# Kernel optimization log

Measured on AMD Instinct MI355X. Metric: run time of the kernel, lower is better.

The kernel has to match this reference:

```python
import jax, jax.numpy as jnp
import numpy as np

B, T = 256, 2048
U = Y = 32
H = 128
Z = 64
L = 2  # GRU layers


def _mlp2(x, w1, b1, w2, b2):
    # Linear -> ReLU -> Linear (PyTorch Linear: y = x @ W.T + b)
    return jax.nn.relu(x @ w1.T + b1) @ w2.T + b2


def _gru_cell(x, h, wih, whh):
    # PyTorch GRUCell (bias=False), gate order [r, z, n]
    gi = x @ wih.T  # [B, 3H]
    gh = h @ whh.T
    i_r, i_z, i_n = jnp.split(gi, 3, axis=-1)
    h_r, h_z, h_n = jnp.split(gh, 3, axis=-1)
    r = jax.nn.sigmoid(i_r + h_r)
    z = jax.nn.sigmoid(i_z + h_z)
    n = jnp.tanh(i_n + r * h_n)
    return (1.0 - z) * n + z * h


def setup_inputs() -> dict:
    key = jax.random.key(0)
    ks = jax.random.split(key, 32)
    f32 = jnp.float32
    w = lambda k, shape: jax.random.normal(k, shape, f32) * 0.05
    inp = {
        'u': jax.random.normal(ks[0], (B, U, T), f32),
        'y': jax.random.normal(ks[1], (B, Y, T), f32),
        'h0': jax.random.uniform(ks[2], (L, B, H), f32),
        # phi_u: Linear(U,H) ReLU Linear(H,H)
        'pu_w1': w(ks[3], (H, U)), 'pu_b1': w(ks[4], (H,)),
        'pu_w2': w(ks[5], (H, H)), 'pu_b2': w(ks[6], (H,)),
        # dynn: Linear(2H,H) ReLU Linear(H,H)
        'dy_w1': w(ks[7], (H, 2 * H)), 'dy_b1': w(ks[8], (H,)),
        'dy_w2': w(ks[9], (H, H)), 'dy_b2': w(ks[10], (H,)),
        # x_mean / x_logvar heads: Linear(H,Z)
        'xm_w': w(ks[11], (Z, H)), 'xm_b': w(ks[12], (Z,)),
        'xlv_w': w(ks[13], (Z, H)), 'xlv_b': w(ks[14], (Z,)),
        # phi_x: Linear(2Z,H) ReLU Linear(H,H)
        'px_w1': w(ks[15], (H, 2 * Z)), 'px_b1': w(ks[16], (H,)),
        'px_w2': w(ks[17], (H, H)), 'px_b2': w(ks[18], (H,)),
        # menn: Linear(H,H) ReLU Linear(H,Y)
        'me_w1': w(ks[19], (H, H)), 'me_b1': w(ks[20], (H,)),
        'me_w2': w(ks[21], (Y, H)), 'me_b2': w(ks[22], (Y,)),
        # GRU (bias=False), stacked per layer: [L, 3H, H]
        'gru_wih': w(ks[23], (L, 3 * H, H)),
        'gru_whh': w(ks[24], (L, 3 * H, H)),
    }
    return inp


def reference(u, y, h0, pu_w1, pu_b1, pu_w2, pu_b2, dy_w1, dy_b1, dy_w2, dy_b2,
              xm_w, xm_b, xlv_w, xlv_b, px_w1, px_b1, px_w2, px_b2,
              me_w1, me_b1, me_w2, me_b2, gru_wih, gru_whh):
    u_seq = jnp.moveaxis(u, 2, 0)  # [T, B, U]
    y_seq = jnp.moveaxis(y, 2, 0)  # [T, B, Y]

    def step(carry, ty):
        h, loss = carry  # h: [L, B, H]
        ut, yt = ty
        phi_u = _mlp2(ut, pu_w1, pu_b1, pu_w2, pu_b2)                     # [B, H]
        dphi = _mlp2(jnp.concatenate([phi_u, h[-1]], axis=1),
                     dy_w1, dy_b1, dy_w2, dy_b2)                          # [B, H]
        x_mean = dphi @ xm_w.T + xm_b                                     # [B, Z]
        x_logvar = dphi @ xlv_w.T + xlv_b                                 # [B, Z]
        # GRU step (uses pre-update h; dynn already consumed old h[-1])
        inp = phi_u
        new_h = []
        for l in range(L):
            hl = _gru_cell(inp, h[l], gru_wih[l], gru_whh[l])
            new_h.append(hl)
            inp = hl
        h = jnp.stack(new_h)
        # mpnt_wt <= 0 branch: pure NN measurement
        phi_x = _mlp2(jnp.concatenate([x_mean, x_logvar], axis=1),
                      px_w1, px_b1, px_w2, px_b2)                         # [B, H]
        y_hat = _mlp2(phi_x, me_w1, me_b1, me_w2, me_b2)                  # [B, Y]
        loss = loss + jnp.sum((y_hat - yt) ** 2)
        return (h, loss), None

    (h, loss), _ = jax.lax.scan(step, (h0, jnp.float32(0.0)), (u_seq, y_seq))
    return loss
```

## Files before the change

kernel.cpp:

```cpp
#include <hip/hip_runtime.h>

#define DI __device__ __forceinline__

typedef unsigned short u16;
typedef unsigned int u32;
typedef unsigned long long u64;
typedef __bf16 bf16v __attribute__((ext_vector_type(8)));
typedef float f32x4 __attribute__((ext_vector_type(4)));

constexpr int B_ = 256, T_ = 2048, H_ = 128;
constexpr int BU = B_ * 32;

constexpr size_t O_PU_W1 = 0;
constexpr size_t O_PU_W2 = 4096;
constexpr size_t O_DY_W1 = 20480;
constexpr size_t O_DY_W2 = 53248;
constexpr size_t O_XM_W  = 69632;
constexpr size_t O_XLV_W = 77824;
constexpr size_t O_PX_W1 = 86016;
constexpr size_t O_PX_W2 = 102400;
constexpr size_t O_ME_W1 = 118784;
constexpr size_t O_ME_W2 = 135168;
constexpr size_t O_WIH   = 139264;
constexpr size_t O_WHH   = 237568;

constexpr size_t WS_WB   = 0;
constexpr size_t WS_HST  = 0x100000;
constexpr size_t WS_PART = 0x140000;
constexpr size_t WS_DATA = 0x180000;

DI u16 f2b(float x) {
  union { float f; unsigned u; } v; v.f = x;
  unsigned r = v.u + 0x7fffu + ((v.u >> 16) & 1u);
  return (u16)(r >> 16);
}
DI float b2f(u16 h) { union { unsigned u; float f; } v; v.u = ((unsigned)h) << 16; return v.f; }
DI float asf(u32 u) { union { unsigned u; float f; } v; v.u = u; return v.f; }
DI float sigm(float x) {
  return __builtin_amdgcn_rcpf(1.f + __builtin_amdgcn_exp2f(-1.44269504f * x));
}
DI float tanhg(float x) {
  return fmaf(2.f, __builtin_amdgcn_rcpf(1.f + __builtin_amdgcn_exp2f(-2.88539008f * x)), -1.f);
}
DI f32x4 MFMA(bf16v a, bf16v b, f32x4 c) {
  return __builtin_amdgcn_mfma_f32_16x16x32_bf16(a, b, c, 0, 0, 0);
}
DI void MFA(f32x4& c, const bf16v& a_agpr, const bf16v& b) {
  asm("v_mfma_f32_16x16x32_bf16 %0, %1, %2, %0"
      : "+v"(c) : "a"(a_agpr), "v"(b));
}
DI bf16v ldb(const u16* p) { return *reinterpret_cast<const bf16v*>(p); }
DI u32 cvtpk(float a, float b) {
  u32 d;
  asm("v_cvt_pk_bf16_f32 %0, %1, %2" : "=v"(d) : "v"(a), "v"(b));
  return d;
}
DI u64 pk4(float a, float b, float c, float d) {
  return (u64)cvtpk(a, b) | ((u64)cvtpk(c, d) << 32);
}
DI void bar_lds() {
  asm volatile("s_waitcnt lgkmcnt(0)\n\ts_barrier" ::: "memory");
}

__global__ void k_convert_weights(
    const float* pu_w1, const float* pu_w2, const float* dy_w1, const float* dy_w2,
    const float* xm_w, const float* xlv_w, const float* px_w1, const float* px_w2,
    const float* me_w1, const float* me_w2, const float* gih, const float* ghh,
    const float* h0, u16* wb, float* hst) {
  int i0 = blockIdx.x * blockDim.x + threadIdx.x;
  int st = gridDim.x * blockDim.x;
#define CVT(src, off, n) for (int i = i0; i < (n); i += st) wb[(off) + i] = f2b(src[i]);
  CVT(pu_w1, O_PU_W1, 4096)  CVT(pu_w2, O_PU_W2, 16384)
  CVT(dy_w1, O_DY_W1, 32768) CVT(dy_w2, O_DY_W2, 16384)
  CVT(xm_w,  O_XM_W,  8192)  CVT(xlv_w, O_XLV_W, 8192)
  CVT(px_w1, O_PX_W1, 16384) CVT(px_w2, O_PX_W2, 16384)
  CVT(me_w1, O_ME_W1, 16384) CVT(me_w2, O_ME_W2, 4096)
  CVT(gih,   O_WIH,   98304) CVT(ghh,   O_WHH,   98304)
#undef CVT
  for (int i = i0; i < 2 * B_ * H_; i += st) hst[i] = h0[i];
}

__global__ void k_transpose(const float* __restrict__ u, const float* __restrict__ y,
                            u16* __restrict__ uT, u16* __restrict__ yT, int t0) {
  const float* src = blockIdx.z ? y : u;
  u16* dst = blockIdx.z ? yT : uT;
  __shared__ float tile[32][33];
  const int tx = threadIdx.x, ty = threadIdx.y;
  const int c0 = blockIdx.x * 32;
  const int r0 = blockIdx.y * 32;
#pragma unroll
  for (int i = 0; i < 4; ++i)
    tile[ty + i * 8][tx] = src[(size_t)(r0 + ty + i * 8) * T_ + t0 + c0 + tx];
  __syncthreads();
#pragma unroll
  for (int i = 0; i < 4; ++i)
    dst[(size_t)(c0 + ty + i * 8) * BU + r0 + tx] = f2b(tile[tx][ty + i * 8]);
}

DI void role_gru(u16* smem, const u16* __restrict__ gi0, const u16* __restrict__ wb,
                 float* __restrict__ hst, u16* __restrict__ h1old, int TCr, int blk) {
  u16* SH0 = smem;
  u16* SH1 = smem + 4352;
  const int lane = threadIdx.x & 63, w = threadIdx.x >> 6;
  const int ln = lane & 15, lq = lane >> 4;
  const int f0 = w * 16;
  const int fme = f0 + lq * 4;
  const int b0 = blk * 16;
  const u16* wh0 = wb + O_WHH;
  const u16* wi1 = wb + O_WIH + 49152;
  const u16* wh1 = wb + O_WHH + 49152;

  bf16v wH0[3][4], wI1[3][4], wH1[3][4];
#pragma unroll
  for (int g = 0; g < 3; ++g)
#pragma unroll
    for (int kt = 0; kt < 4; ++kt) {
      size_t row = (size_t)(g * 128 + f0 + ln);
      size_t col = (size_t)kt * 32 + lq * 8;
      wH0[g][kt] = ldb(wh0 + row * H_ + col);
      wI1[g][kt] = ldb(wi1 + row * H_ + col);
      wH1[g][kt] = ldb(wh1 + row * H_ + col);
    }
#pragma unroll
  for (int g = 0; g < 3; ++g)
#pragma unroll
    for (int kt = 0; kt < 4; ++kt)
      asm volatile("" : "+a"(wH0[g][kt]), "+a"(wI1[g][kt]), "+a"(wH1[g][kt]));

  float h0s[4], h1s[4];
#pragma unroll
  for (int j = 0; j < 4; ++j) {
    h0s[j] = hst[(size_t)(0 * B_ + b0 + ln) * H_ + fme + j];
    h1s[j] = hst[(size_t)(1 * B_ + b0 + ln) * H_ + fme + j];
  }
  *reinterpret_cast<u64*>(&SH0[ln * 136 + fme]) = pk4(h0s[0], h0s[1], h0s[2], h0s[3]);
  *reinterpret_cast<u64*>(&SH1[ln * 136 + fme]) = pk4(h1s[0], h1s[1], h1s[2], h1s[3]);
  u16* hp = h1old + (size_t)(b0 + ln) * H_ + fme;
  *reinterpret_cast<u64*>(hp) = pk4(h1s[0], h1s[1], h1s[2], h1s[3]);

  const u16* gp = gi0 + (size_t)(b0 + ln) * 384 + fme;
  u64 gq0 = *reinterpret_cast<const u64*>(gp);
  u64 gq1 = *reinterpret_cast<const u64*>(gp + 128);
  u64 gq2 = *reinterpret_cast<const u64*>(gp + 256);
  gp += (size_t)B_ * 384;

  __syncthreads();

#define GRU_STEP(CUR, NXT, T)                                                   \
  {                                                                             \
    u16* H0c = SH0 + (CUR) * 2176; u16* H0n = SH0 + (NXT) * 2176;               \
    u16* H1c = SH1 + (CUR) * 2176; u16* H1n = SH1 + (NXT) * 2176;               \
    f32x4 cR = {0,0,0,0}, cZ = {0,0,0,0}, cHN = {0,0,0,0};                      \
    _Pragma("unroll")                                                           \
    for (int kt = 0; kt < 4; ++kt) {                                            \
      bf16v aH = ldb(&H0c[ln * 136 + kt * 32 + lq * 8]);                        \
      MFA(cR,  wH0[0][kt], aH);                                                 \
      MFA(cZ,  wH0[1][kt], aH);                                                 \
      MFA(cHN, wH0[2][kt], aH);                                                 \
    }                                                                           \
    {                                                                           \
      u32 l0 = (u32)gq0, h0w = (u32)(gq0 >> 32);                                \
      u32 l1 = (u32)gq1, h1w = (u32)(gq1 >> 32);                                \
      u32 l2 = (u32)gq2, h2w = (u32)(gq2 >> 32);                                \
      float gr[4] = {asf(l0 << 16), asf(l0 & 0xffff0000u),                      \
                     asf(h0w << 16), asf(h0w & 0xffff0000u)};                   \
      float gz[4] = {asf(l1 << 16), asf(l1 & 0xffff0000u),                      \
                     asf(h1w << 16), asf(h1w & 0xffff0000u)};                   \
      float gn[4] = {asf(l2 << 16), asf(l2 & 0xffff0000u),                      \
                     asf(h2w << 16), asf(h2w & 0xffff0000u)};                   \
      _Pragma("unroll")                                                         \
      for (int j = 0; j < 4; ++j) {                                             \
        float r = sigm(cR[j] + gr[j]);                                          \
        float z = sigm(cZ[j] + gz[j]);                                          \
        float n = tanhg(fmaf(r, cHN[j], gn[j]));                                \
        h0s[j] = fmaf(z, h0s[j] - n, n);                                        \
      }                                                                         \
      *reinterpret_cast<u64*>(&H0n[ln * 136 + fme]) =                           \
          pk4(h0s[0], h0s[1], h0s[2], h0s[3]);                                  \
    }                                                                           \
    bar_lds();                         \
    if ((T) + 1 < TCr) {                                                        \
      gq0 = *reinterpret_cast<const u64*>(gp);                                  \
      gq1 = *reinterpret_cast<const u64*>(gp + 128);                            \
      gq2 = *reinterpret_cast<const u64*>(gp + 256);                            \
      gp += (size_t)B_ * 384;                                                   \
    }                                                                           \
    f32x4 dR = {0,0,0,0}, dZ = {0,0,0,0}, dIN = {0,0,0,0}, dHN = {0,0,0,0};     \
    _Pragma("unroll")                                                           \
    for (int kt = 0; kt < 4; ++kt) {                                            \
      bf16v aI  = ldb(&H0n[ln * 136 + kt * 32 + lq * 8]);                       \
      bf16v aH1 = ldb(&H1c[ln * 136 + kt * 32 + lq * 8]);                       \
      MFA(dR,  wI1[0][kt], aI);                                                 \
      MFA(dR,  wH1[0][kt], aH1);                                                \
      MFA(dZ,  wI1[1][kt], aI);                                                 \
      MFA(dZ,  wH1[1][kt], aH1);                                                \
      MFA(dIN, wI1[2][kt], aI);                                                 \
      MFA(dHN, wH1[2][kt], aH1);                                                \
    }                                                                           \
    {                                                                           \
      _Pragma("unroll")                                                         \
      for (int j = 0; j < 4; ++j) {                                             \
        float r = sigm(dR[j]);                                                  \
        float z = sigm(dZ[j]);                                                  \
        float n = tanhg(fmaf(r, dHN[j], dIN[j]));                               \
        h1s[j] = fmaf(z, h1s[j] - n, n);                                        \
      }                                                                         \
      u64 q = pk4(h1s[0], h1s[1], h1s[2], h1s[3]);                              \
      *reinterpret_cast<u64*>(&H1n[ln * 136 + fme]) = q;                        \
      if ((T) + 1 < TCr) {                                                      \
        hp += (size_t)B_ * H_;                                                  \
        *reinterpret_cast<u64*>(hp) = q;                                        \
      }                                                                         \
    }                                                                           \
  }

  for (int tt = 0; tt < TCr; tt += 2) {
    GRU_STEP(0, 1, tt)
    GRU_STEP(1, 0, tt + 1)
  }
#undef GRU_STEP

#pragma unroll
  for (int j = 0; j < 4; ++j) {
    hst[(size_t)(0 * B_ + b0 + ln) * H_ + fme + j] = h0s[j];
    hst[(size_t)(1 * B_ + b0 + ln) * H_ + fme + j] = h1s[j];
  }
}

DI void layer128(const u16* __restrict__ W, const float* __restrict__ bias,
                 const u16* A, u16* Dst, int dstOff, int nTiles, bool relu,
                 int ln, int lq) {
  bf16v a[2][4];
#pragma unroll
  for (int mt = 0; mt < 2; ++mt)
#pragma unroll
    for (int kt = 0; kt < 4; ++kt)
      a[mt][kt] = ldb(A + (mt * 16 + ln) * 136 + kt * 32 + lq * 8);
  for (int nt = 0; nt < nTiles; ++nt) {
    f32x4 c0 = {0,0,0,0}, c1 = {0,0,0,0};
#pragma unroll
    for (int kt = 0; kt < 4; ++kt) {
      bf16v b = ldb(W + (nt * 16 + ln) * 128 + kt * 32 + lq * 8);
      c0 = MFMA(a[0][kt], b, c0); c1 = MFMA(a[1][kt], b, c1);
    }
    float bv = bias[nt * 16 + ln];
#pragma unroll
    for (int mt = 0; mt < 2; ++mt)
#pragma unroll
      for (int j = 0; j < 4; ++j) {
        float v = (mt ? c1[j] : c0[j]) + bv;
        if (relu) v = fmaxf(v, 0.f);
        Dst[(mt * 16 + lq * 4 + j) * 136 + dstOff + nt * 16 + ln] = f2b(v);
      }
  }
}

DI void role_post(u16* smem, const u16* __restrict__ phiu, const u16* __restrict__ h1old,
                  const u16* __restrict__ yT, const u16* __restrict__ wb,
                  const float* dy_b1, const float* dy_b2, const float* xm_b,
                  const float* xlv_b, const float* px_b1, const float* px_b2,
                  const float* me_b1, const float* me_b2,
                  float* __restrict__ partials, int first, int blk) {
  const int lane = threadIdx.x & 63, w = threadIdx.x >> 6;
  const int ln = lane & 15, lq = lane >> 4;
  const int r0 = (blk * 8 + w) * 32;
  u16* X = smem + w * 8704;
  u16* Yb = X + 4352;
  float* wsum = (float*)(smem + 69632);

  {
    bf16v a[2][8];
#pragma unroll
    for (int mt = 0; mt < 2; ++mt)
#pragma unroll
      for (int kt = 0; kt < 8; ++kt) {
        size_t row = (size_t)(r0 + mt * 16 + ln);
        a[mt][kt] = (kt < 4) ? ldb(phiu + row * H_ + kt * 32 + lq * 8)
                             : ldb(h1old + row * H_ + (kt - 4) * 32 + lq * 8);
      }
    const u16* W = wb + O_DY_W1;
    for (int nt = 0; nt < 8; ++nt) {
      f32x4 c0 = {0,0,0,0}, c1 = {0,0,0,0};
#pragma unroll
      for (int kt = 0; kt < 8; ++kt) {
        bf16v b = ldb(W + (nt * 16 + ln) * 256 + kt * 32 + lq * 8);
        c0 = MFMA(a[0][kt], b, c0); c1 = MFMA(a[1][kt], b, c1);
      }
      float bv = dy_b1[nt * 16 + ln];
#pragma unroll
      for (int mt = 0; mt < 2; ++mt)
#pragma unroll
        for (int j = 0; j < 4; ++j) {
          float v = (mt ? c1[j] : c0[j]) + bv;
          X[(mt * 16 + lq * 4 + j) * 136 + nt * 16 + ln] = f2b(fmaxf(v, 0.f));
        }
    }
  }
  layer128(wb + O_DY_W2, dy_b2, X, Yb, 0, 8, false, ln, lq);
  layer128(wb + O_XM_W,  xm_b,  Yb, X, 0, 4, false, ln, lq);
  layer128(wb + O_XLV_W, xlv_b, Yb, X, 64, 4, false, ln, lq);
  layer128(wb + O_PX_W1, px_b1, X, Yb, 0, 8, true,  ln, lq);
  layer128(wb + O_PX_W2, px_b2, Yb, X, 0, 8, false, ln, lq);
  layer128(wb + O_ME_W1, me_b1, X, Yb, 0, 8, true,  ln, lq);

  float lsum = 0.f;
  {
    bf16v a[2][4];
#pragma unroll
    for (int mt = 0; mt < 2; ++mt)
#pragma unroll
      for (int kt = 0; kt < 4; ++kt)
        a[mt][kt] = ldb(Yb + (mt * 16 + ln) * 136 + kt * 32 + lq * 8);
    const u16* W = wb + O_ME_W2;
#pragma unroll
    for (int nt = 0; nt < 2; ++nt) {
      f32x4 c0 = {0,0,0,0}, c1 = {0,0,0,0};
#pragma unroll
      for (int kt = 0; kt < 4; ++kt) {
        bf16v b = ldb(W + (nt * 16 + ln) * 128 + kt * 32 + lq * 8);
        c0 = MFMA(a[0][kt], b, c0); c1 = MFMA(a[1][kt], b, c1);
      }
      float bv = me_b2[nt * 16 + ln];
#pragma unroll
      for (int mt = 0; mt < 2; ++mt)
#pragma unroll
        for (int j = 0; j < 4; ++j) {
          int m = mt * 16 + lq * 4 + j;
          float v = (mt ? c1[j] : c0[j]) + bv;
          float yv = b2f(yT[(size_t)(r0 + m) * 32 + nt * 16 + ln]);
          float d = v - yv;
          lsum += d * d;
        }
    }
  }
#pragma unroll
  for (int o = 32; o; o >>= 1) lsum += __shfl_down(lsum, o);
  if (lane == 0) wsum[w] = lsum;
  __syncthreads();
  if (threadIdx.x == 0) {
    float v = 0.f;
#pragma unroll
    for (int i = 0; i < 8; ++i) v += wsum[i];
    if (first) partials[blk] = v;
    else       partials[blk] += v;
  }
}

DI void role_phiu(u16* smem, const u16* __restrict__ uT, const u16* __restrict__ wb,
                  const float* __restrict__ pu_b1, const float* __restrict__ pu_b2,
                  u16* __restrict__ phiu, u16* __restrict__ gi0, int blk) {
  const int lane = threadIdx.x & 63, w = threadIdx.x >> 6;
  const int ln = lane & 15, lq = lane >> 4;
  const int r0 = (blk * 8 + w) * 32;
  u16* hb  = smem + w * 4352;
  u16* hb2 = smem + 34816 + w * 4352;

  bf16v a0 = ldb(uT + (size_t)(r0 + ln) * 32 + lq * 8);
  bf16v a1 = ldb(uT + (size_t)(r0 + 16 + ln) * 32 + lq * 8);
  const u16* w1 = wb + O_PU_W1;
#pragma unroll
  for (int nt = 0; nt < 8; ++nt) {
    f32x4 c0 = {0.f, 0.f, 0.f, 0.f}, c1 = {0.f, 0.f, 0.f, 0.f};
    bf16v b = ldb(w1 + (nt * 16 + ln) * 32 + lq * 8);
    c0 = MFMA(a0, b, c0); c1 = MFMA(a1, b, c1);
    float bv = pu_b1[nt * 16 + ln];
#pragma unroll
    for (int j = 0; j < 4; ++j) {
      hb[(lq * 4 + j) * 136 + nt * 16 + ln]      = f2b(fmaxf(c0[j] + bv, 0.f));
      hb[(16 + lq * 4 + j) * 136 + nt * 16 + ln] = f2b(fmaxf(c1[j] + bv, 0.f));
    }
  }
  bf16v a[2][4];
#pragma unroll
  for (int mt = 0; mt < 2; ++mt)
#pragma unroll
    for (int kt = 0; kt < 4; ++kt)
      a[mt][kt] = ldb(hb + (mt * 16 + ln) * 136 + kt * 32 + lq * 8);
  const u16* w2 = wb + O_PU_W2;
#pragma unroll
  for (int nt = 0; nt < 8; ++nt) {
    f32x4 c0 = {0.f, 0.f, 0.f, 0.f}, c1 = {0.f, 0.f, 0.f, 0.f};
#pragma unroll
    for (int kt = 0; kt < 4; ++kt) {
      bf16v b = ldb(w2 + (nt * 16 + ln) * 128 + kt * 32 + lq * 8);
      c0 = MFMA(a[0][kt], b, c0); c1 = MFMA(a[1][kt], b, c1);
    }
    float bv = pu_b2[nt * 16 + ln];
#pragma unroll
    for (int mt = 0; mt < 2; ++mt)
#pragma unroll
      for (int j = 0; j < 4; ++j) {
        float v = (mt ? c1[j] : c0[j]) + bv;
        hb2[(mt * 16 + lq * 4 + j) * 136 + nt * 16 + ln] = f2b(v);
      }
  }
  __syncthreads();

#pragma unroll
  for (int i = 0; i < 16; ++i) {
    int idx = lane + 64 * i;
    int row = idx >> 5, c4 = idx & 31;
    u64 v = *reinterpret_cast<const u64*>(&hb2[row * 136 + c4 * 4]);
    *reinterpret_cast<u64*>(&phiu[(size_t)(r0 + row) * 128 + c4 * 4]) = v;
  }

  bf16v bP[2][4];
#pragma unroll
  for (int bh = 0; bh < 2; ++bh)
#pragma unroll
    for (int kt = 0; kt < 4; ++kt)
      bP[bh][kt] = ldb(&hb2[(bh * 16 + ln) * 136 + kt * 32 + lq * 8]);
  const u16* wih0 = wb + O_WIH;
  for (int nt = 0; nt < 24; ++nt) {
    bf16v aW[4];
#pragma unroll
    for (int kt = 0; kt < 4; ++kt)
      aW[kt] = ldb(wih0 + (size_t)(nt * 16 + ln) * 128 + kt * 32 + lq * 8);
#pragma unroll
    for (int bh = 0; bh < 2; ++bh) {
      f32x4 c = {0.f, 0.f, 0.f, 0.f};
#pragma unroll
      for (int kt = 0; kt < 4; ++kt) c = MFMA(aW[kt], bP[bh][kt], c);
      u64 q = pk4(c[0], c[1], c[2], c[3]);
      *reinterpret_cast<u64*>(
          &gi0[(size_t)(r0 + bh * 16 + ln) * 384 + nt * 16 + lq * 4]) = q;
    }
  }
}

DI void role_transpose(u16* smem, const float* __restrict__ u, const float* __restrict__ y,
                       u16* __restrict__ uT, u16* __restrict__ yT, int t0, int blk, int TCr) {
  float* tile = (float*)smem;
  const int worker = threadIdx.x >> 8;
  const int tid = threadIdx.x & 255;
  const int tx = tid & 31, ty = tid >> 5;
  float* tl = tile + worker * (32 * 33);
  const int ntt = TCr / 32;
  for (int i = 0; i < 4; ++i) {
    int gtile = blk * 8 + worker * 4 + i;
    int tt = gtile % ntt;
    int rest = gtile / ntt;
    int rr = rest & 255, uy = rest >> 8;
    const float* src = uy ? y : u;
    u16* dst = uy ? yT : uT;
    int c0 = tt * 32, r0 = rr * 32;
#pragma unroll
    for (int k = 0; k < 4; ++k)
      tl[(ty + k * 8) * 33 + tx] = src[(size_t)(r0 + ty + k * 8) * T_ + t0 + c0 + tx];
    __syncthreads();
#pragma unroll
    for (int k = 0; k < 4; ++k)
      dst[(size_t)(c0 + ty + k * 8) * BU + r0 + tx] = f2b(tl[tx * 33 + ty + k * 8]);
    __syncthreads();
  }
}

__global__ __launch_bounds__(512, 2) void k_mega(
    const float* u, const float* yy,
    const u16* uT_r, u16* uT_w, u16* yT_w, const u16* yT_r,
    const u16* phiu_r, u16* phiu_w,
    const u16* gi0_r, u16* gi0_w,
    const u16* h1_r, u16* h1_w,
    const u16* wb, float* hst,
    const float* pu_b1, const float* pu_b2,
    const float* dy_b1, const float* dy_b2, const float* xm_b, const float* xlv_b,
    const float* px_b1, const float* px_b2, const float* me_b1, const float* me_b2,
    float* partials, int first,
    int TCr, int nG, int nP, int nU, int t0T) {
  __shared__ __align__(16) u16 smem[69664];
  int b = blockIdx.x;
  if (b < nG) { role_gru(smem, gi0_r, wb, hst, h1_w, TCr, b); return; }
  b -= nG;
  if (b < nP) {
    role_post(smem, phiu_r, h1_r, yT_r, wb, dy_b1, dy_b2, xm_b, xlv_b,
              px_b1, px_b2, me_b1, me_b2, partials, first, b);
    return;
  }
  b -= nP;
  if (b < nU) { role_phiu(smem, uT_r, wb, pu_b1, pu_b2, phiu_w, gi0_w, b); return; }
  b -= nU;
  role_transpose(smem, u, yy, uT_w, yT_w, t0T, b, TCr);
}

__global__ void k_finalize(const float* __restrict__ partials, float* __restrict__ out,
                           int nPart) {
  __shared__ double s[256];
  double acc = 0.0;
  for (int i = threadIdx.x; i < nPart; i += 256) acc += (double)partials[i];
  s[threadIdx.x] = acc;
  __syncthreads();
  for (int o = 128; o; o >>= 1) {
    if (threadIdx.x < o) s[threadIdx.x] += s[threadIdx.x + o];
    __syncthreads();
  }
  if (threadIdx.x == 0) out[0] = (float)s[0];
}

extern "C" void kernel_launch(void* const* d_in, const int* in_sizes, int n_in,
                              void* d_out, int out_size, void* d_ws, size_t ws_size,
                              hipStream_t stream) {
  const float* u     = (const float*)d_in[0];
  const float* y     = (const float*)d_in[1];
  const float* h0    = (const float*)d_in[2];
  const float* pu_w1 = (const float*)d_in[3];
  const float* pu_b1 = (const float*)d_in[4];
  const float* pu_w2 = (const float*)d_in[5];
  const float* pu_b2 = (const float*)d_in[6];
  const float* dy_w1 = (const float*)d_in[7];
  const float* dy_b1 = (const float*)d_in[8];
  const float* dy_w2 = (const float*)d_in[9];
  const float* dy_b2 = (const float*)d_in[10];
  const float* xm_w  = (const float*)d_in[11];
  const float* xm_b  = (const float*)d_in[12];
  const float* xlv_w = (const float*)d_in[13];
  const float* xlv_b = (const float*)d_in[14];
  const float* px_w1 = (const float*)d_in[15];
  const float* px_b1 = (const float*)d_in[16];
  const float* px_w2 = (const float*)d_in[17];
  const float* px_b2 = (const float*)d_in[18];
  const float* me_w1 = (const float*)d_in[19];
  const float* me_b1 = (const float*)d_in[20];
  const float* me_w2 = (const float*)d_in[21];
  const float* me_b2 = (const float*)d_in[22];
  const float* gih   = (const float*)d_in[23];
  const float* ghh   = (const float*)d_in[24];

  int TC = 64;
  for (int cand : {256, 128}) {
    size_t ut = (size_t)cand * B_ * 32 * 2;
    size_t ph = (size_t)cand * B_ * 128 * 2;
    size_t gi = (size_t)cand * B_ * 384 * 2;
    if (WS_DATA + 6 * ut + 5 * ph + 2 * gi <= ws_size) { TC = cand; break; }
  }
  const int NCH = T_ / TC;
  const int RC = TC * B_;
  size_t ut_b = (size_t)RC * 32 * 2, ph_b = (size_t)RC * 128 * 2, gi_b = (size_t)RC * 384 * 2;

  char* ws = (char*)d_ws;
  u16* wb    = (u16*)(ws + WS_WB);
  float* hst = (float*)(ws + WS_HST);
  float* prt = (float*)(ws + WS_PART);
  char* p = ws + WS_DATA;
  u16* uTb[2]; u16* yTb[4]; u16* phb[3]; u16* h1b[2]; u16* gib[2];
  for (int i = 0; i < 2; ++i) { uTb[i] = (u16*)p; p += ut_b; }
  for (int i = 0; i < 4; ++i) { yTb[i] = (u16*)p; p += ut_b; }
  for (int i = 0; i < 3; ++i) { phb[i] = (u16*)p; p += ph_b; }
  for (int i = 0; i < 2; ++i) { h1b[i] = (u16*)p; p += ph_b; }
  for (int i = 0; i < 2; ++i) { gib[i] = (u16*)p; p += gi_b; }
  float* out = (float*)d_out;

  const int nPostB = RC / 256;
  const int nPhiB  = RC / 256;
  const int nTrB   = (TC / 32) * 64;

  k_convert_weights<<<256, 256, 0, stream>>>(pu_w1, pu_w2, dy_w1, dy_w2, xm_w, xlv_w,
                                             px_w1, px_w2, me_w1, me_w2, gih, ghh,
                                             h0, wb, hst);
  k_transpose<<<dim3(TC / 32, 256, 2), dim3(32, 8), 0, stream>>>(u, y, uTb[0], yTb[0], 0);
  if (NCH > 1)
    k_transpose<<<dim3(TC / 32, 256, 2), dim3(32, 8), 0, stream>>>(u, y, uTb[1], yTb[1], TC);
  k_mega<<<nPhiB, 512, 0, stream>>>(u, y, uTb[0], uTb[0], yTb[0], yTb[0],
                                    phb[0], phb[0], gib[0], gib[0], h1b[0], h1b[0],
                                    wb, hst, pu_b1, pu_b2, dy_b1, dy_b2, xm_b, xlv_b,
                                    px_b1, px_b2, me_b1, me_b2, prt, 0,
                                    TC, 0, 0, nPhiB, 0);
  for (int c = 0; c <= NCH; ++c) {
    int nG = (c < NCH) ? 16 : 0;
    int nP = (c >= 1) ? nPostB : 0;
    int nU = (c + 1 < NCH) ? nPhiB : 0;
    int nT = (c + 2 < NCH) ? nTrB : 0;
    int grid = nG + nP + nU + nT;
    if (!grid) continue;
    k_mega<<<grid, 512, 0, stream>>>(
        u, y,
        uTb[(c + 1) & 1], uTb[(c + 2) & 1], yTb[(c + 2) & 3],
        yTb[c >= 1 ? (c - 1) & 3 : 0],
        phb[c >= 1 ? (c - 1) % 3 : 0], phb[(c + 1) % 3],
        gib[c & 1], gib[(c + 1) & 1],
        h1b[c >= 1 ? (c - 1) & 1 : 0], h1b[c & 1],
        wb, hst, pu_b1, pu_b2, dy_b1, dy_b2, xm_b, xlv_b,
        px_b1, px_b2, me_b1, me_b2,
        prt, (c == 1) ? 1 : 0,
        TC, nG, nP, nU, (c + 2) * TC);
  }
  k_finalize<<<1, 256, 0, stream>>>(prt, out, nPostB);
}
```

Before: 3.063 ms.

## Skew GRU layers so layer-1 step t overlaps layer-0 step t+1

Restructures the two-layer GRU recurrence as a wavefront pipeline. A prologue computes layer-0 step 0, and each later period computes layer-1 step s-1 and layer-0 step s from the same loaded h0 fragments. This removes one LDS barrier per timestep and reuses the A-operand loads for both layers' MFMAs. In exchange the double-buffer slot indexing and boundary conditions become more intricate, and correctness depends on handling the tail and odd TCr cases properly.

```diff
diff --git a/kernel.cpp b/kernel.cpp
--- a/kernel.cpp
+++ b/kernel.cpp
@@ -133,8 +133,8 @@
     h0s[j] = hst[(size_t)(0 * B_ + b0 + ln) * H_ + fme + j];
     h1s[j] = hst[(size_t)(1 * B_ + b0 + ln) * H_ + fme + j];
   }
-  *reinterpret_cast<u64*>(&SH0[ln * 136 + fme]) = pk4(h0s[0], h0s[1], h0s[2], h0s[3]);
-  *reinterpret_cast<u64*>(&SH1[ln * 136 + fme]) = pk4(h1s[0], h1s[1], h1s[2], h1s[3]);
+  *reinterpret_cast<u64*>(&SH0[2176 + ln * 136 + fme]) = pk4(h0s[0], h0s[1], h0s[2], h0s[3]);
+  *reinterpret_cast<u64*>(&SH1[2176 + ln * 136 + fme]) = pk4(h1s[0], h1s[1], h1s[2], h1s[3]);
   u16* hp = h1old + (size_t)(b0 + ln) * H_ + fme;
   *reinterpret_cast<u64*>(hp) = pk4(h1s[0], h1s[1], h1s[2], h1s[3]);
 
@@ -146,19 +146,60 @@
 
   __syncthreads();
 
-#define GRU_STEP(CUR, NXT, T)                                                   \
+  {
+    f32x4 cR = {0,0,0,0}, cZ = {0,0,0,0}, cHN = {0,0,0,0};
+#pragma unroll
+    for (int kt = 0; kt < 4; ++kt) {
+      bf16v aH = ldb(&SH0[2176 + ln * 136 + kt * 32 + lq * 8]);
+      MFA(cR,  wH0[0][kt], aH);
+      MFA(cZ,  wH0[1][kt], aH);
+      MFA(cHN, wH0[2][kt], aH);
+    }
+    u32 l0 = (u32)gq0, h0w = (u32)(gq0 >> 32);
+    u32 l1 = (u32)gq1, h1w = (u32)(gq1 >> 32);
+    u32 l2 = (u32)gq2, h2w = (u32)(gq2 >> 32);
+    float gr[4] = {asf(l0 << 16), asf(l0 & 0xffff0000u), asf(h0w << 16), asf(h0w & 0xffff0000u)};
+    float gz[4] = {asf(l1 << 16), asf(l1 & 0xffff0000u), asf(h1w << 16), asf(h1w & 0xffff0000u)};
+    float gn[4] = {asf(l2 << 16), asf(l2 & 0xffff0000u), asf(h2w << 16), asf(h2w & 0xffff0000u)};
+#pragma unroll
+    for (int j = 0; j < 4; ++j) {
+      float r = sigm(cR[j] + gr[j]);
+      float z = sigm(cZ[j] + gz[j]);
+      float n = tanhg(fmaf(r, cHN[j], gn[j]));
+      h0s[j] = fmaf(z, h0s[j] - n, n);
+    }
+    *reinterpret_cast<u64*>(&SH0[0 * 2176 + ln * 136 + fme]) =
+        pk4(h0s[0], h0s[1], h0s[2], h0s[3]);
+    gq0 = *reinterpret_cast<const u64*>(gp);
+    gq1 = *reinterpret_cast<const u64*>(gp + 128);
+    gq2 = *reinterpret_cast<const u64*>(gp + 256);
+    gp += (size_t)B_ * 384;
+    bar_lds();
+  }
+
+#define GRU_PERIOD(H0R, H0W, DOL0, SLOT_OK, PF)                                 \
   {                                                                             \
-    u16* H0c = SH0 + (CUR) * 2176; u16* H0n = SH0 + (NXT) * 2176;               \
-    u16* H1c = SH1 + (CUR) * 2176; u16* H1n = SH1 + (NXT) * 2176;               \
-    f32x4 cR = {0,0,0,0}, cZ = {0,0,0,0}, cHN = {0,0,0,0};                      \
+    bf16v aH[4], aG[4];                                                         \
     _Pragma("unroll")                                                           \
     for (int kt = 0; kt < 4; ++kt) {                                            \
-      bf16v aH = ldb(&H0c[ln * 136 + kt * 32 + lq * 8]);                        \
-      MFA(cR,  wH0[0][kt], aH);                                                 \
-      MFA(cZ,  wH0[1][kt], aH);                                                 \
-      MFA(cHN, wH0[2][kt], aH);                                                 \
+      aH[kt] = ldb(&SH0[(H0R) * 2176 + ln * 136 + kt * 32 + lq * 8]);           \
+      aG[kt] = ldb(&SH1[(H0W) * 2176 + ln * 136 + kt * 32 + lq * 8]);           \
     }                                                                           \
-    {                                                                           \
+    f32x4 dR = {0,0,0,0}, dZ = {0,0,0,0}, dIN = {0,0,0,0}, dHN = {0,0,0,0};     \
+    _Pragma("unroll")                                                           \
+    for (int kt = 0; kt < 4; ++kt) {                                            \
+      MFA(dR,  wI1[0][kt], aH[kt]);  MFA(dR,  wH1[0][kt], aG[kt]);              \
+      MFA(dZ,  wI1[1][kt], aH[kt]);  MFA(dZ,  wH1[1][kt], aG[kt]);              \
+      MFA(dIN, wI1[2][kt], aH[kt]);  MFA(dHN, wH1[2][kt], aG[kt]);              \
+    }                                                                           \
+    if (DOL0) {                                                                 \
+      f32x4 cR = {0,0,0,0}, cZ = {0,0,0,0}, cHN = {0,0,0,0};                    \
+      _Pragma("unroll")                                                         \
+      for (int kt = 0; kt < 4; ++kt) {                                          \
+        MFA(cR,  wH0[0][kt], aH[kt]);                                           \
+        MFA(cZ,  wH0[1][kt], aH[kt]);                                           \
+        MFA(cHN, wH0[2][kt], aH[kt]);                                           \
+      }                                                                         \
       u32 l0 = (u32)gq0, h0w = (u32)(gq0 >> 32);                                \
       u32 l1 = (u32)gq1, h1w = (u32)(gq1 >> 32);                                \
       u32 l2 = (u32)gq2, h2w = (u32)(gq2 >> 32);                                \
@@ -175,27 +216,8 @@
         float n = tanhg(fmaf(r, cHN[j], gn[j]));                                \
         h0s[j] = fmaf(z, h0s[j] - n, n);                                        \
       }                                                                         \
-      *reinterpret_cast<u64*>(&H0n[ln * 136 + fme]) =                           \
+      *reinterpret_cast<u64*>(&SH0[(H0W) * 2176 + ln * 136 + fme]) =            \
           pk4(h0s[0], h0s[1], h0s[2], h0s[3]);                                  \
-    }                                                                           \
-    bar_lds();                         \
-    if ((T) + 1 < TCr) {                                                        \
-      gq0 = *reinterpret_cast<const u64*>(gp);                                  \
-      gq1 = *reinterpret_cast<const u64*>(gp + 128);                            \
-      gq2 = *reinterpret_cast<const u64*>(gp + 256);                            \
-      gp += (size_t)B_ * 384;                                                   \
-    }                                                                           \
-    f32x4 dR = {0,0,0,0}, dZ = {0,0,0,0}, dIN = {0,0,0,0}, dHN = {0,0,0,0};     \
-    _Pragma("unroll")                                                           \
-    for (int kt = 0; kt < 4; ++kt) {                                            \
-      bf16v aI  = ldb(&H0n[ln * 136 + kt * 32 + lq * 8]);                       \
-      bf16v aH1 = ldb(&H1c[ln * 136 + kt * 32 + lq * 8]);                       \
-      MFA(dR,  wI1[0][kt], aI);                                                 \
-      MFA(dR,  wH1[0][kt], aH1);                                                \
-      MFA(dZ,  wI1[1][kt], aI);                                                 \
-      MFA(dZ,  wH1[1][kt], aH1);                                                \
-      MFA(dIN, wI1[2][kt], aI);                                                 \
-      MFA(dHN, wH1[2][kt], aH1);                                                \
     }                                                                           \
     {                                                                           \
       _Pragma("unroll")                                                         \
@@ -206,19 +228,26 @@
         h1s[j] = fmaf(z, h1s[j] - n, n);                                        \
       }                                                                         \
       u64 q = pk4(h1s[0], h1s[1], h1s[2], h1s[3]);                              \
-      *reinterpret_cast<u64*>(&H1n[ln * 136 + fme]) = q;                        \
-      if ((T) + 1 < TCr) {                                                      \
+      *reinterpret_cast<u64*>(&SH1[(H0R) * 2176 + ln * 136 + fme]) = q;         \
+      if (SLOT_OK) {                                                            \
         hp += (size_t)B_ * H_;                                                  \
         *reinterpret_cast<u64*>(hp) = q;                                        \
       }                                                                         \
     }                                                                           \
-  }
-
-  for (int tt = 0; tt < TCr; tt += 2) {
-    GRU_STEP(0, 1, tt)
-    GRU_STEP(1, 0, tt + 1)
-  }
-#undef GRU_STEP
+    if (PF) {                                                                   \
+      gq0 = *reinterpret_cast<const u64*>(gp);                                  \
+      gq1 = *reinterpret_cast<const u64*>(gp + 128);                            \
+      gq2 = *reinterpret_cast<const u64*>(gp + 256);                            \
+      gp += (size_t)B_ * 384;                                                   \
+    }                                                                           \
+    bar_lds();                                                                  \
+  }
+
+  for (int s = 1; s <= TCr; s += 2) {
+    GRU_PERIOD(0, 1, true, true, (s + 1 < TCr))
+    GRU_PERIOD(1, 0, (s + 1 < TCr), (s + 1 < TCr), (s + 2 < TCr))
+  }
+#undef GRU_PERIOD
 
 #pragma unroll
   for (int j = 0; j < 4; ++j) {
```

Result: faster. 2.752 ms, median of 2 (-10.1%).

## Software-pipeline the two GRU layers across timesteps with skewed stages

Applied to the files above, without the earlier changes.

Restructures the recurrent GRU loop so that layer 1 at step s-1 runs in the same stage as layer 0 at step s. Layer 0's hidden-state operands are reused as layer 1's input, and the gi bias is folded into the accumulator init. The aim is to overlap the two layers' MFMA chains and elementwise work, shortening the serial critical path per timestep. In exchange it adds a second barrier per stage, prologue and epilogue guards, and more complex double-buffer indexing that could introduce bugs.

```diff
diff --git a/kernel.cpp b/kernel.cpp
--- a/kernel.cpp
+++ b/kernel.cpp
@@ -133,8 +133,8 @@
     h0s[j] = hst[(size_t)(0 * B_ + b0 + ln) * H_ + fme + j];
     h1s[j] = hst[(size_t)(1 * B_ + b0 + ln) * H_ + fme + j];
   }
-  *reinterpret_cast<u64*>(&SH0[ln * 136 + fme]) = pk4(h0s[0], h0s[1], h0s[2], h0s[3]);
-  *reinterpret_cast<u64*>(&SH1[ln * 136 + fme]) = pk4(h1s[0], h1s[1], h1s[2], h1s[3]);
+  *reinterpret_cast<u64*>(&SH0[2176 + ln * 136 + fme]) = pk4(h0s[0], h0s[1], h0s[2], h0s[3]);
+  *reinterpret_cast<u64*>(&SH1[2176 + ln * 136 + fme]) = pk4(h1s[0], h1s[1], h1s[2], h1s[3]);
   u16* hp = h1old + (size_t)(b0 + ln) * H_ + fme;
   *reinterpret_cast<u64*>(hp) = pk4(h1s[0], h1s[1], h1s[2], h1s[3]);
 
@@ -144,60 +144,40 @@
   u64 gq2 = *reinterpret_cast<const u64*>(gp + 256);
   gp += (size_t)B_ * 384;
 
+  bf16v aH0[4];
+  f32x4 cR, cZ, cHN;
+  f32x4 dR, dZ, dIN, dHN;
+  float gn[4];
+
   __syncthreads();
 
-#define GRU_STEP(CUR, NXT, T)                                                   \
+#define GRU_AB(S, PM1, P)                                                       \
   {                                                                             \
-    u16* H0c = SH0 + (CUR) * 2176; u16* H0n = SH0 + (NXT) * 2176;               \
-    u16* H1c = SH1 + (CUR) * 2176; u16* H1n = SH1 + (NXT) * 2176;               \
-    f32x4 cR = {0,0,0,0}, cZ = {0,0,0,0}, cHN = {0,0,0,0};                      \
-    _Pragma("unroll")                                                           \
-    for (int kt = 0; kt < 4; ++kt) {                                            \
-      bf16v aH = ldb(&H0c[ln * 136 + kt * 32 + lq * 8]);                        \
-      MFA(cR,  wH0[0][kt], aH);                                                 \
-      MFA(cZ,  wH0[1][kt], aH);                                                 \
-      MFA(cHN, wH0[2][kt], aH);                                                 \
+                                                      \
+    if ((S) <= TCr) {                                                           \
+      _Pragma("unroll")                                                         \
+      for (int kt = 0; kt < 4; ++kt)                                            \
+        aH0[kt] = ldb(&SH0[(PM1) * 2176 + ln * 136 + kt * 32 + lq * 8]);        \
     }                                                                           \
-    {                                                                           \
+    if ((S) < TCr) {                                                            \
       u32 l0 = (u32)gq0, h0w = (u32)(gq0 >> 32);                                \
       u32 l1 = (u32)gq1, h1w = (u32)(gq1 >> 32);                                \
       u32 l2 = (u32)gq2, h2w = (u32)(gq2 >> 32);                                \
-      float gr[4] = {asf(l0 << 16), asf(l0 & 0xffff0000u),                      \
-                     asf(h0w << 16), asf(h0w & 0xffff0000u)};                   \
-      float gz[4] = {asf(l1 << 16), asf(l1 & 0xffff0000u),                      \
-                     asf(h1w << 16), asf(h1w & 0xffff0000u)};                   \
-      float gn[4] = {asf(l2 << 16), asf(l2 & 0xffff0000u),                      \
-                     asf(h2w << 16), asf(h2w & 0xffff0000u)};                   \
+      cR = f32x4{asf(l0 << 16), asf(l0 & 0xffff0000u),                          \
+                 asf(h0w << 16), asf(h0w & 0xffff0000u)};                       \
+      cZ = f32x4{asf(l1 << 16), asf(l1 & 0xffff0000u),                          \
+                 asf(h1w << 16), asf(h1w & 0xffff0000u)};                       \
+      gn[0] = asf(l2 << 16); gn[1] = asf(l2 & 0xffff0000u);                     \
+      gn[2] = asf(h2w << 16); gn[3] = asf(h2w & 0xffff0000u);                   \
+      cHN = f32x4{0, 0, 0, 0};                                                  \
       _Pragma("unroll")                                                         \
-      for (int j = 0; j < 4; ++j) {                                             \
-        float r = sigm(cR[j] + gr[j]);                                          \
-        float z = sigm(cZ[j] + gz[j]);                                          \
-        float n = tanhg(fmaf(r, cHN[j], gn[j]));                                \
-        h0s[j] = fmaf(z, h0s[j] - n, n);                                        \
+      for (int kt = 0; kt < 4; ++kt) {                                          \
+        MFA(cR,  wH0[0][kt], aH0[kt]);                                          \
+        MFA(cZ,  wH0[1][kt], aH0[kt]);                                          \
+        MFA(cHN, wH0[2][kt], aH0[kt]);                                          \
       }                                                                         \
-      *reinterpret_cast<u64*>(&H0n[ln * 136 + fme]) =                           \
-          pk4(h0s[0], h0s[1], h0s[2], h0s[3]);                                  \
     }                                                                           \
-    bar_lds();                         \
-    if ((T) + 1 < TCr) {                                                        \
-      gq0 = *reinterpret_cast<const u64*>(gp);                                  \
-      gq1 = *reinterpret_cast<const u64*>(gp + 128);                            \
-      gq2 = *reinterpret_cast<const u64*>(gp + 256);                            \
-      gp += (size_t)B_ * 384;                                                   \
-    }                                                                           \
-    f32x4 dR = {0,0,0,0}, dZ = {0,0,0,0}, dIN = {0,0,0,0}, dHN = {0,0,0,0};     \
-    _Pragma("unroll")                                                           \
-    for (int kt = 0; kt < 4; ++kt) {                                            \
-      bf16v aI  = ldb(&H0n[ln * 136 + kt * 32 + lq * 8]);                       \
-      bf16v aH1 = ldb(&H1c[ln * 136 + kt * 32 + lq * 8]);                       \
-      MFA(dR,  wI1[0][kt], aI);                                                 \
-      MFA(dR,  wH1[0][kt], aH1);                                                \
-      MFA(dZ,  wI1[1][kt], aI);                                                 \
-      MFA(dZ,  wH1[1][kt], aH1);                                                \
-      MFA(dIN, wI1[2][kt], aI);                                                 \
-      MFA(dHN, wH1[2][kt], aH1);                                                \
-    }                                                                           \
-    {                                                                           \
+    if ((S) >= 2) {               \
       _Pragma("unroll")                                                         \
       for (int j = 0; j < 4; ++j) {                                             \
         float r = sigm(dR[j]);                                                  \
@@ -206,19 +186,56 @@
         h1s[j] = fmaf(z, h1s[j] - n, n);                                        \
       }                                                                         \
       u64 q = pk4(h1s[0], h1s[1], h1s[2], h1s[3]);                              \
-      *reinterpret_cast<u64*>(&H1n[ln * 136 + fme]) = q;                        \
-      if ((T) + 1 < TCr) {                                                      \
+      *reinterpret_cast<u64*>(&SH1[(P) * 2176 + ln * 136 + fme]) = q;           \
+      if ((S) <= TCr) {                                                         \
         hp += (size_t)B_ * H_;                                                  \
-        *reinterpret_cast<u64*>(hp) = q;                                        \
+        *reinterpret_cast<u64*>(hp) = q;                    \
       }                                                                         \
     }                                                                           \
-  }
-
-  for (int tt = 0; tt < TCr; tt += 2) {
-    GRU_STEP(0, 1, tt)
-    GRU_STEP(1, 0, tt + 1)
-  }
-#undef GRU_STEP
+    bar_lds();                                                                  \
+                                                      \
+    if ((S) >= 1 && (S) <= TCr) {                       \
+      dR = f32x4{0,0,0,0}; dZ = f32x4{0,0,0,0};                                 \
+      dIN = f32x4{0,0,0,0}; dHN = f32x4{0,0,0,0};                               \
+      _Pragma("unroll")                                                         \
+      for (int kt = 0; kt < 4; ++kt) {      \
+        MFA(dR,  wI1[0][kt], aH0[kt]);                                          \
+        MFA(dZ,  wI1[1][kt], aH0[kt]);                                          \
+        MFA(dIN, wI1[2][kt], aH0[kt]);                                          \
+      }                                                                         \
+      _Pragma("unroll")                                                         \
+      for (int kt = 0; kt < 4; ++kt) {      \
+        bf16v aG = ldb(&SH1[(P) * 2176 + ln * 136 + kt * 32 + lq * 8]);         \
+        MFA(dR,  wH1[0][kt], aG);                                               \
+        MFA(dZ,  wH1[1][kt], aG);                                               \
+        MFA(dHN, wH1[2][kt], aG);                                               \
+      }                                                                         \
+    }                                                                           \
+    if ((S) < TCr) {                  \
+      _Pragma("unroll")                                                         \
+      for (int j = 0; j < 4; ++j) {                                             \
+        float r = sigm(cR[j]);                                                  \
+        float z = sigm(cZ[j]);                                                  \
+        float n = tanhg(fmaf(r, cHN[j], gn[j]));                                \
+        h0s[j] = fmaf(z, h0s[j] - n, n);                                        \
+      }                                                                         \
+      *reinterpret_cast<u64*>(&SH0[(P) * 2176 + ln * 136 + fme]) =              \
+          pk4(h0s[0], h0s[1], h0s[2], h0s[3]);                                  \
+      if ((S) + 1 < TCr) {                                                      \
+        gq0 = *reinterpret_cast<const u64*>(gp);                                \
+        gq1 = *reinterpret_cast<const u64*>(gp + 128);                          \
+        gq2 = *reinterpret_cast<const u64*>(gp + 256);                          \
+        gp += (size_t)B_ * 384;                                                 \
+      }                                                                         \
+    }                                                                           \
+    bar_lds();                                                                  \
+  }
+
+  for (int s = 0; s <= TCr; s += 2) {
+    GRU_AB(s, 1, 0)
+    GRU_AB(s + 1, 0, 1)
+  }
+#undef GRU_AB
 
 #pragma unroll
   for (int j = 0; j < 4; ++j) {
```

New measurement: 3.562 ms. 1.16x slower.
